# Kernel optimization log

Measured on AMD Instinct MI355X. Metric: run time of the kernel, lower is better.

Reference implementation:

```python
import jax, jax.numpy as jnp
import numpy as np

N, P, D, C = 8192, 512, 2, 4   # queries, coeff grid points, spatial dim, num coefficients
HA = 32                        # attention_net hidden
HP, CP = 32, 16                # pointswise_mlp hidden / output
HG = 256                       # green_function_net hidden


def setup_inputs() -> dict:
    key = jax.random.key(0)
    ks = jax.random.split(key, 16)
    g = lambda k, shp, s: jax.random.normal(k, shp, dtype=jnp.float32) * s
    return {
        "r": g(ks[0], (N, 2 * D), 1.0),
        "r_prime": g(ks[1], (N, 2 * D), 1.0),
        "coeff_x": g(ks[2], (P, D), 1.0),
        "coeff_y": g(ks[3], (P, C), 1.0),
        # attention_net MLP (no bias): concat(q,k)=4 -> 32 -> 32 -> 1
        "Wa1": g(ks[4], (2 * D, HA), 0.5),
        "Wa2": g(ks[5], (HA, HA), 1.0 / np.sqrt(HA)),
        "Wa3": g(ks[6], (HA, 1), 1.0 / np.sqrt(HA)),
        # pointswise_mlp: C -> 32 -> 16
        "Wp1": g(ks[7], (C, HP), 0.5), "bp1": jnp.zeros((HP,), jnp.float32),
        "Wp2": g(ks[8], (HP, CP), 1.0 / np.sqrt(HP)), "bp2": jnp.zeros((CP,), jnp.float32),
        # green_function_net: 4+4+16=24 -> 256 -> 256 -> 1 (exp at the end)
        "Wg1": g(ks[9], (2 * D + 2 * D + CP, HG), 1.0 / np.sqrt(24.0)), "bg1": jnp.zeros((HG,), jnp.float32),
        "Wg2": g(ks[10], (HG, HG), 1.0 / np.sqrt(HG)), "bg2": jnp.zeros((HG,), jnp.float32),
        "Wg3": g(ks[11], (HG, 1), 0.1 / np.sqrt(HG)), "bg3": jnp.zeros((1,), jnp.float32),
    }


def reference(r, r_prime, coeff_x, coeff_y,
              Wa1, Wa2, Wa3, Wp1, bp1, Wp2, bp2,
              Wg1, bg1, Wg2, bg2, Wg3, bg3):
    # --- CoefficientNet: pairwise MLP attention over the coefficient grid ---
    q = r[:, :D]  # (N, 2) spatial position only
    # first layer of attn MLP on concat([q, k]) split into q- and k- parts
    h = jax.nn.relu(q @ Wa1[:D][None if False else slice(None)]  # (N, HA)
                    [..., :] [..., :]  # no-op for readability
                    if False else (q @ Wa1[:D])[:, None, :] + (coeff_x @ Wa1[D:])[None, :, :])  # (N, P, HA)
    h = jax.nn.relu(h @ Wa2)                     # (N, P, HA)
    logits = (h @ Wa3)[..., 0]                   # (N, P)
    attn = jax.nn.softmax(logits, axis=-1)       # (N, P)
    attn_out = attn @ coeff_y                    # (N, C)
    c = jax.nn.relu(attn_out @ Wp1 + bp1) @ Wp2 + bp2  # (N, CP)
    # --- GreenFunctionNet ---
    x = jnp.concatenate([r, r_prime, c], axis=-1)       # (N, 24)
    g1 = jax.nn.relu(x @ Wg1 + bg1)
    g2 = jax.nn.relu(g1 @ Wg2 + bg2)
    return jnp.exp(g2 @ Wg3 + bg3)                      # (N, 1)
```

## Files before the change

kernel.cpp:

```cpp
#include <hip/hip_runtime.h>
#include <math.h>

#define N_ 8192
#define P_ 512

typedef __fp16 half8  __attribute__((ext_vector_type(8)));
typedef __fp16 half2t __attribute__((ext_vector_type(2)));
typedef float  floatx16 __attribute__((ext_vector_type(16)));

union H8 { half8 v; half2t h2[4]; };

static __device__ __forceinline__ half2t pk2(float a, float b) {
    return __builtin_amdgcn_cvt_pkrtz(a, b);
}

#define HP_OFF 17408
#define XS_OFF 21760

__global__ __launch_bounds__(512, 2) void k_fused(
    const float* __restrict__ r,
    const float* __restrict__ rp,
    const float* __restrict__ coeff_x,
    const float* __restrict__ coeff_y,
    const float* __restrict__ Wa1,
    const float* __restrict__ Wa2,
    const float* __restrict__ Wa3,
    const float* __restrict__ Wp1,
    const float* __restrict__ bp1,
    const float* __restrict__ Wp2,
    const float* __restrict__ bp2,
    const float* __restrict__ Wg1,
    const float* __restrict__ bg1,
    const float* __restrict__ Wg2,
    const float* __restrict__ bg2,
    const float* __restrict__ Wg3,
    const float* __restrict__ bg3,
    float* __restrict__ out)
{
    __shared__ __align__(16) unsigned char reg0[49152];
    __shared__ float sA[8][32];
    __shared__ float aoA[4][8][32];
    __shared__ float aoS[32][4];

    const int tid  = threadIdx.x;
    const int n0   = blockIdx.x * 32;
    const int lane = tid & 63;
    const int wv   = tid >> 6;
    const int j32  = lane & 31;
    const int hl   = lane >> 5;
    const int k0g  = hl * 8;

    {
        const float2 cx = ((const float2*)coeff_x)[tid];
        half2t* wrow = (half2t*)(reg0 + tid * 96);
#pragma unroll
        for (int q = 0; q < 16; ++q) {
            const float b0 = cx.x * Wa1[64 + 2*q]     + cx.y * Wa1[96 + 2*q];
            const float b1 = cx.x * Wa1[64 + 2*q + 1] + cx.y * Wa1[96 + 2*q + 1];
            wrow[q] = pk2(b0, b1);
        }
    }

    half2t anh1[4], anh2[4];
    {
        const float2 rv = ((const float2*)r)[2 * (n0 + j32)];
#pragma unroll
        for (int q = 0; q < 4; ++q) {
            const int k1 = k0g + 2*q, k2 = 16 + k0g + 2*q;
            anh1[q] = pk2(rv.x*Wa1[k1]   + rv.y*Wa1[32+k1],
                          rv.x*Wa1[k1+1] + rv.y*Wa1[32+k1+1]);
            anh2[q] = pk2(rv.x*Wa1[k2]   + rv.y*Wa1[32+k2],
                          rv.x*Wa1[k2+1] + rv.y*Wa1[32+k2+1]);
        }
    }
    H8 af1, af2;
#pragma unroll
    for (int q = 0; q < 4; ++q) {
        af1.h2[q] = pk2(Wa2[(k0g + 2*q)     * 32 + j32],
                        Wa2[(k0g + 2*q + 1) * 32 + j32]);
        af2.h2[q] = pk2(Wa2[(16 + k0g + 2*q)     * 32 + j32],
                        Wa2[(16 + k0g + 2*q + 1) * 32 + j32]);
    }
    float w3[16];
#pragma unroll
    for (int g = 0; g < 4; ++g)
#pragma unroll
        for (int i = 0; i < 4; ++i)
            w3[g*4 + i] = Wa3[g*8 + 4*hl + i];

    __syncthreads();

    const half2t zero2 = pk2(0.f, 0.f);
    float s = 0.0f, aox = 0.f, aoy = 0.f, aoz = 0.f, aow = 0.f;

#pragma unroll 2
    for (int pl = 0; pl < 64; ++pl) {
        const int ploc = wv * 64 + pl;
        const half2t* rowq = (const half2t*)(reg0 + ploc * 96) + hl * 4;

        H8 bf1, bf2;
#pragma unroll
        for (int q = 0; q < 4; ++q) {
            bf1.h2[q] = __builtin_elementwise_max(anh1[q] + rowq[q],     zero2);
            bf2.h2[q] = __builtin_elementwise_max(anh2[q] + rowq[8 + q], zero2);
        }

        floatx16 zc = {};
        floatx16 acc = __builtin_amdgcn_mfma_f32_32x32x16_f16(af1.v, bf1.v, zc, 0, 0, 0);
        acc = __builtin_amdgcn_mfma_f32_32x32x16_f16(af2.v, bf2.v, acc, 0, 0, 0);

        float d0 = 0.f, d1 = 0.f, d2 = 0.f, d3 = 0.f;
#pragma unroll
        for (int i = 0; i < 4; ++i) {
            d0 += fmaxf(acc[i],      0.f) * w3[i];
            d1 += fmaxf(acc[4 + i],  0.f) * w3[4 + i];
            d2 += fmaxf(acc[8 + i],  0.f) * w3[8 + i];
            d3 += fmaxf(acc[12 + i], 0.f) * w3[12 + i];
        }
        float dot = (d0 + d1) + (d2 + d3);
        dot += __shfl_xor(dot, 32);

        const float e = __expf(dot);
        const float4 cyv = ((const float4*)coeff_y)[ploc];
        s   += e;
        aox += e * cyv.x;
        aoy += e * cyv.y;
        aoz += e * cyv.z;
        aow += e * cyv.w;
    }

    if (lane < 32) {
        sA[wv][lane]      = s;
        aoA[0][wv][lane]  = aox;
        aoA[1][wv][lane]  = aoy;
        aoA[2][wv][lane]  = aoz;
        aoA[3][wv][lane]  = aow;
    }
    __syncthreads();

    if (tid < 32) {
        float S = 0.f, A0 = 0.f, A1 = 0.f, A2 = 0.f, A3 = 0.f;
#pragma unroll
        for (int w = 0; w < 8; ++w) {
            S  += sA[w][tid];
            A0 += aoA[0][w][tid];
            A1 += aoA[1][w][tid];
            A2 += aoA[2][w][tid];
            A3 += aoA[3][w][tid];
        }
        const float inv = 1.0f / S;
        aoS[tid][0] = A0 * inv;
        aoS[tid][1] = A1 * inv;
        aoS[tid][2] = A2 * inv;
        aoS[tid][3] = A3 * inv;
    }
    __syncthreads();

    float* hpS = (float*)(reg0 + HP_OFF);
    float* xS  = (float*)(reg0 + XS_OFF);
    const int nB = tid & 31;
    const int iB = tid >> 5;

    if (tid < 256) {
        const int nn = tid >> 3, k = tid & 7;
        xS[nn*25 + k] = (k < 4) ? r[(n0+nn)*4 + k] : rp[(n0+nn)*4 + k - 4];
    }
    {
        const float a0 = aoS[nB][0], a1 = aoS[nB][1], a2 = aoS[nB][2], a3 = aoS[nB][3];
#pragma unroll
        for (int rep = 0; rep < 2; ++rep) {
            const int i = iB + rep*16;
            float a = bp1[i] + a0*Wp1[i] + a1*Wp1[32+i] + a2*Wp1[64+i] + a3*Wp1[96+i];
            hpS[nB*33 + i] = fmaxf(a, 0.0f);
        }
    }
    __syncthreads();

    {
        float a = bp2[iB];
#pragma unroll
        for (int i = 0; i < 32; ++i) a += hpS[nB*33 + i] * Wp2[i*16 + iB];
        xS[nB*25 + 8 + iB] = a;
    }
    __syncthreads();

    const int jcol = (wv << 5) + j32;
    __fp16* g1S = (__fp16*)reg0;

    {
        H8 xa1, xa2, wb1, wb2;
        const float* xrow = xS + j32 * 25;
#pragma unroll
        for (int q = 0; q < 4; ++q) {
            xa1.h2[q] = pk2(xrow[k0g + 2*q], xrow[k0g + 2*q + 1]);
            wb1.h2[q] = pk2(Wg1[(k0g + 2*q)*256 + jcol],
                            Wg1[(k0g + 2*q + 1)*256 + jcol]);
            if (hl == 0) {
                xa2.h2[q] = pk2(xrow[16 + 2*q], xrow[16 + 2*q + 1]);
                wb2.h2[q] = pk2(Wg1[(16 + 2*q)*256 + jcol],
                                Wg1[(17 + 2*q)*256 + jcol]);
            } else {
                xa2.h2[q] = pk2(0.f, 0.f);
                wb2.h2[q] = pk2(0.f, 0.f);
            }
        }
        floatx16 g1acc = {};
        g1acc = __builtin_amdgcn_mfma_f32_32x32x16_f16(xa1.v, wb1.v, g1acc, 0, 0, 0);
        g1acc = __builtin_amdgcn_mfma_f32_32x32x16_f16(xa2.v, wb2.v, g1acc, 0, 0, 0);

        const float b1v = bg1[jcol];
#pragma unroll
        for (int i = 0; i < 16; ++i) {
            const int row = (i & 3) + 8*(i >> 2) + 4*hl;
            g1S[row*264 + jcol] = (__fp16)fmaxf(g1acc[i] + b1v, 0.0f);
        }
    }
    __syncthreads();

    {
        H8 wB[16];
#pragma unroll
        for (int kk = 0; kk < 16; ++kk) {
            const int kb = kk*16 + hl*8;
#pragma unroll
            for (int q = 0; q < 4; ++q)
                wB[kk].h2[q] = pk2(Wg2[(kb + 2*q)*256 + jcol],
                                   Wg2[(kb + 2*q + 1)*256 + jcol]);
        }
        floatx16 acc2 = {};
        const __fp16* arow = g1S + j32 * 264;
#pragma unroll
        for (int kk = 0; kk < 16; ++kk) {
            H8 af;
            af.v = *(const half8*)(arow + kk*16 + hl*8);
            acc2 = __builtin_amdgcn_mfma_f32_32x32x16_f16(af.v, wB[kk].v, acc2, 0, 0, 0);
        }

        const float b2v = bg2[jcol];
        const float w3v = Wg3[jcol];
        float part[16];
#pragma unroll
        for (int i = 0; i < 16; ++i)
            part[i] = fmaxf(acc2[i] + b2v, 0.0f) * w3v;
#pragma unroll
        for (int off = 1; off <= 16; off <<= 1) {
#pragma unroll
            for (int i = 0; i < 16; ++i) part[i] += __shfl_xor(part[i], off);
        }
        float* redS = &sA[0][0];
        if ((lane & 31) == 0) {
#pragma unroll
            for (int i = 0; i < 16; ++i) {
                const int row = (i & 3) + 8*(i >> 2) + 4*hl;
                redS[wv*32 + row] = part[i];
            }
        }
        __syncthreads();

        if (tid < 32) {
            float v = bg3[0];
#pragma unroll
            for (int w = 0; w < 8; ++w) v += redS[w*32 + tid];
            out[n0 + tid] = __expf(v);
        }
    }
}

extern "C" void kernel_launch(void* const* d_in, const int* in_sizes, int n_in,
                              void* d_out, int out_size, void* d_ws, size_t ws_size,
                              hipStream_t stream)
{
    const float* r   = (const float*)d_in[0];
    const float* rp  = (const float*)d_in[1];
    const float* cx  = (const float*)d_in[2];
    const float* cy  = (const float*)d_in[3];
    const float* Wa1 = (const float*)d_in[4];
    const float* Wa2 = (const float*)d_in[5];
    const float* Wa3 = (const float*)d_in[6];
    const float* Wp1 = (const float*)d_in[7];
    const float* bp1 = (const float*)d_in[8];
    const float* Wp2 = (const float*)d_in[9];
    const float* bp2 = (const float*)d_in[10];
    const float* Wg1 = (const float*)d_in[11];
    const float* bg1 = (const float*)d_in[12];
    const float* Wg2 = (const float*)d_in[13];
    const float* bg2 = (const float*)d_in[14];
    const float* Wg3 = (const float*)d_in[15];
    const float* bg3 = (const float*)d_in[16];

    hipLaunchKernelGGL(k_fused, dim3(N_/32), dim3(512), 0, stream,
                       r, rp, cx, cy, Wa1, Wa2, Wa3, Wp1, bp1, Wp2, bp2,
                       Wg1, bg1, Wg2, bg2, Wg3, bg3, (float*)d_out);
}
```

Baseline: 112.9 us.

## Split fused kernel into attention and MLP kernels with P-split atomics

Splits the single fused kernel into an attention kernel that divides the 512 coefficient points across two blocks per query tile and combines partial softmax sums with global atomics, followed by a separate kernel for the pointwise and green-function MLPs. This doubles the attention grid to 512 blocks to raise occupancy and parallelism on the CU array. It also caches coeff_y in shared memory and replaces the final attention projection with packed fp16 dot2 instructions. The cost is an extra memset, an extra launch, global atomics, and lower precision in the logit dot product. Partials use unnormalised exp without max subtraction, as before.

```diff
diff --git a/kernel.cpp b/kernel.cpp
--- a/kernel.cpp
+++ b/kernel.cpp
@@ -14,17 +14,148 @@
     return __builtin_amdgcn_cvt_pkrtz(a, b);
 }
 
-#define HP_OFF 17408
-#define XS_OFF 21760
-
-__global__ __launch_bounds__(512, 2) void k_fused(
+__global__ __launch_bounds__(512, 2) void k_attn(
     const float* __restrict__ r,
-    const float* __restrict__ rp,
     const float* __restrict__ coeff_x,
     const float* __restrict__ coeff_y,
     const float* __restrict__ Wa1,
     const float* __restrict__ Wa2,
     const float* __restrict__ Wa3,
+    float* __restrict__ ws_s,
+    float* __restrict__ ws_ao)
+{
+    __shared__ __align__(16) unsigned char bpS[256 * 96];
+    __shared__ __align__(16) float4 cyS[256];
+    __shared__ float sA[8][32];
+    __shared__ float aoA[4][8][32];
+
+    const int tid    = threadIdx.x;
+    const int ntile  = blockIdx.x >> 1;
+    const int pblock = (blockIdx.x & 1) * 256;
+    const int n0     = ntile * 32;
+    const int lane   = tid & 63;
+    const int wv     = tid >> 6;
+    const int j32    = lane & 31;
+    const int hl     = lane >> 5;
+    const int k0g    = hl * 8;
+
+    if (tid < 256) {
+        const float2 cx = ((const float2*)coeff_x)[pblock + tid];
+        half2t* wrow = (half2t*)(bpS + tid * 96);
+#pragma unroll
+        for (int q = 0; q < 16; ++q) {
+            const float b0 = cx.x * Wa1[64 + 2*q]     + cx.y * Wa1[96 + 2*q];
+            const float b1 = cx.x * Wa1[64 + 2*q + 1] + cx.y * Wa1[96 + 2*q + 1];
+            wrow[q] = pk2(b0, b1);
+        }
+    } else {
+        cyS[tid - 256] = ((const float4*)coeff_y)[pblock + tid - 256];
+    }
+
+    half2t anh1[4], anh2[4];
+    {
+        const float2 rv = ((const float2*)r)[2 * (n0 + j32)];
+#pragma unroll
+        for (int q = 0; q < 4; ++q) {
+            const int k1 = k0g + 2*q, k2 = 16 + k0g + 2*q;
+            anh1[q] = pk2(rv.x*Wa1[k1]   + rv.y*Wa1[32+k1],
+                          rv.x*Wa1[k1+1] + rv.y*Wa1[32+k1+1]);
+            anh2[q] = pk2(rv.x*Wa1[k2]   + rv.y*Wa1[32+k2],
+                          rv.x*Wa1[k2+1] + rv.y*Wa1[32+k2+1]);
+        }
+    }
+    H8 af1, af2;
+#pragma unroll
+    for (int q = 0; q < 4; ++q) {
+        af1.h2[q] = pk2(Wa2[(k0g + 2*q)     * 32 + j32],
+                        Wa2[(k0g + 2*q + 1) * 32 + j32]);
+        af2.h2[q] = pk2(Wa2[(16 + k0g + 2*q)     * 32 + j32],
+                        Wa2[(16 + k0g + 2*q + 1) * 32 + j32]);
+    }
+    half2t w3h[8];
+#pragma unroll
+    for (int q = 0; q < 8; ++q) {
+        const int r0 = ((2*q) & 3) + 8*(q >> 1) + 4*hl;
+        w3h[q] = pk2(Wa3[r0], Wa3[r0 + 1]);
+    }
+
+    __syncthreads();
+
+    const half2t zero2 = pk2(0.f, 0.f);
+    float s = 0.0f, aox = 0.f, aoy = 0.f, aoz = 0.f, aow = 0.f;
+
+#pragma unroll 2
+    for (int pl = 0; pl < 32; ++pl) {
+        const int ploc = wv * 32 + pl;
+        const half2t* rowq = (const half2t*)(bpS + ploc * 96) + hl * 4;
+
+        H8 bf1, bf2;
+#pragma unroll
+        for (int q = 0; q < 4; ++q) {
+            bf1.h2[q] = __builtin_elementwise_max(anh1[q] + rowq[q],     zero2);
+            bf2.h2[q] = __builtin_elementwise_max(anh2[q] + rowq[8 + q], zero2);
+        }
+
+        floatx16 zc = {};
+        floatx16 acc = __builtin_amdgcn_mfma_f32_32x32x16_f16(af1.v, bf1.v, zc, 0, 0, 0);
+        acc = __builtin_amdgcn_mfma_f32_32x32x16_f16(af2.v, bf2.v, acc, 0, 0, 0);
+
+        float d0 = 0.f, d1 = 0.f;
+#pragma unroll
+        for (int q = 0; q < 8; q += 2) {
+            half2t z0 = __builtin_elementwise_max(pk2(acc[2*q],   acc[2*q+1]), zero2);
+            half2t z1 = __builtin_elementwise_max(pk2(acc[2*q+2], acc[2*q+3]), zero2);
+            d0 = __builtin_amdgcn_fdot2(z0, w3h[q],   d0, false);
+            d1 = __builtin_amdgcn_fdot2(z1, w3h[q+1], d1, false);
+        }
+        float dot = d0 + d1;
+        dot += __shfl_xor(dot, 32);
+
+        const float e = __expf(dot);
+        const float4 cyv = cyS[ploc];
+        s   += e;
+        aox += e * cyv.x;
+        aoy += e * cyv.y;
+        aoz += e * cyv.z;
+        aow += e * cyv.w;
+    }
+
+    if (lane < 32) {
+        sA[wv][lane]      = s;
+        aoA[0][wv][lane]  = aox;
+        aoA[1][wv][lane]  = aoy;
+        aoA[2][wv][lane]  = aoz;
+        aoA[3][wv][lane]  = aow;
+    }
+    __syncthreads();
+
+    if (tid < 32) {
+        float S = 0.f, A0 = 0.f, A1 = 0.f, A2 = 0.f, A3 = 0.f;
+#pragma unroll
+        for (int w = 0; w < 8; ++w) {
+            S  += sA[w][tid];
+            A0 += aoA[0][w][tid];
+            A1 += aoA[1][w][tid];
+            A2 += aoA[2][w][tid];
+            A3 += aoA[3][w][tid];
+        }
+        const int n = n0 + tid;
+        atomicAdd(ws_s + n, S);
+        atomicAdd(ws_ao + n*4 + 0, A0);
+        atomicAdd(ws_ao + n*4 + 1, A1);
+        atomicAdd(ws_ao + n*4 + 2, A2);
+        atomicAdd(ws_ao + n*4 + 3, A3);
+    }
+}
+
+#define HP_OFF 17408
+#define XS_OFF 21760
+
+__global__ __launch_bounds__(512) void k_rest(
+    const float* __restrict__ r,
+    const float* __restrict__ rp,
+    const float* __restrict__ ws_s,
+    const float* __restrict__ ws_ao,
     const float* __restrict__ Wp1,
     const float* __restrict__ bp1,
     const float* __restrict__ Wp2,
@@ -37,9 +168,8 @@
     const float* __restrict__ bg3,
     float* __restrict__ out)
 {
-    __shared__ __align__(16) unsigned char reg0[49152];
-    __shared__ float sA[8][32];
-    __shared__ float aoA[4][8][32];
+    __shared__ __align__(16) unsigned char reg0[25984];
+    __shared__ float redS[8][32];
     __shared__ float aoS[32][4];
 
     const int tid  = threadIdx.x;
@@ -50,121 +180,23 @@
     const int hl   = lane >> 5;
     const int k0g  = hl * 8;
 
-    {
-        const float2 cx = ((const float2*)coeff_x)[tid];
-        half2t* wrow = (half2t*)(reg0 + tid * 96);
-#pragma unroll
-        for (int q = 0; q < 16; ++q) {
-            const float b0 = cx.x * Wa1[64 + 2*q]     + cx.y * Wa1[96 + 2*q];
-            const float b1 = cx.x * Wa1[64 + 2*q + 1] + cx.y * Wa1[96 + 2*q + 1];
-            wrow[q] = pk2(b0, b1);
-        }
-    }
-
-    half2t anh1[4], anh2[4];
-    {
-        const float2 rv = ((const float2*)r)[2 * (n0 + j32)];
-#pragma unroll
-        for (int q = 0; q < 4; ++q) {
-            const int k1 = k0g + 2*q, k2 = 16 + k0g + 2*q;
-            anh1[q] = pk2(rv.x*Wa1[k1]   + rv.y*Wa1[32+k1],
-                          rv.x*Wa1[k1+1] + rv.y*Wa1[32+k1+1]);
-            anh2[q] = pk2(rv.x*Wa1[k2]   + rv.y*Wa1[32+k2],
-                          rv.x*Wa1[k2+1] + rv.y*Wa1[32+k2+1]);
-        }
-    }
-    H8 af1, af2;
-#pragma unroll
-    for (int q = 0; q < 4; ++q) {
-        af1.h2[q] = pk2(Wa2[(k0g + 2*q)     * 32 + j32],
-                        Wa2[(k0g + 2*q + 1) * 32 + j32]);
-        af2.h2[q] = pk2(Wa2[(16 + k0g + 2*q)     * 32 + j32],
-                        Wa2[(16 + k0g + 2*q + 1) * 32 + j32]);
-    }
-    float w3[16];
-#pragma unroll
-    for (int g = 0; g < 4; ++g)
-#pragma unroll
-        for (int i = 0; i < 4; ++i)
-            w3[g*4 + i] = Wa3[g*8 + 4*hl + i];
-
-    __syncthreads();
-
-    const half2t zero2 = pk2(0.f, 0.f);
-    float s = 0.0f, aox = 0.f, aoy = 0.f, aoz = 0.f, aow = 0.f;
-
-#pragma unroll 2
-    for (int pl = 0; pl < 64; ++pl) {
-        const int ploc = wv * 64 + pl;
-        const half2t* rowq = (const half2t*)(reg0 + ploc * 96) + hl * 4;
-
-        H8 bf1, bf2;
-#pragma unroll
-        for (int q = 0; q < 4; ++q) {
-            bf1.h2[q] = __builtin_elementwise_max(anh1[q] + rowq[q],     zero2);
-            bf2.h2[q] = __builtin_elementwise_max(anh2[q] + rowq[8 + q], zero2);
-        }
-
-        floatx16 zc = {};
-        floatx16 acc = __builtin_amdgcn_mfma_f32_32x32x16_f16(af1.v, bf1.v, zc, 0, 0, 0);
-        acc = __builtin_amdgcn_mfma_f32_32x32x16_f16(af2.v, bf2.v, acc, 0, 0, 0);
-
-        float d0 = 0.f, d1 = 0.f, d2 = 0.f, d3 = 0.f;
-#pragma unroll
-        for (int i = 0; i < 4; ++i) {
-            d0 += fmaxf(acc[i],      0.f) * w3[i];
-            d1 += fmaxf(acc[4 + i],  0.f) * w3[4 + i];
-            d2 += fmaxf(acc[8 + i],  0.f) * w3[8 + i];
-            d3 += fmaxf(acc[12 + i], 0.f) * w3[12 + i];
-        }
-        float dot = (d0 + d1) + (d2 + d3);
-        dot += __shfl_xor(dot, 32);
-
-        const float e = __expf(dot);
-        const float4 cyv = ((const float4*)coeff_y)[ploc];
-        s   += e;
-        aox += e * cyv.x;
-        aoy += e * cyv.y;
-        aoz += e * cyv.z;
-        aow += e * cyv.w;
-    }
-
-    if (lane < 32) {
-        sA[wv][lane]      = s;
-        aoA[0][wv][lane]  = aox;
-        aoA[1][wv][lane]  = aoy;
-        aoA[2][wv][lane]  = aoz;
-        aoA[3][wv][lane]  = aow;
-    }
-    __syncthreads();
-
-    if (tid < 32) {
-        float S = 0.f, A0 = 0.f, A1 = 0.f, A2 = 0.f, A3 = 0.f;
-#pragma unroll
-        for (int w = 0; w < 8; ++w) {
-            S  += sA[w][tid];
-            A0 += aoA[0][w][tid];
-            A1 += aoA[1][w][tid];
-            A2 += aoA[2][w][tid];
-            A3 += aoA[3][w][tid];
-        }
-        const float inv = 1.0f / S;
-        aoS[tid][0] = A0 * inv;
-        aoS[tid][1] = A1 * inv;
-        aoS[tid][2] = A2 * inv;
-        aoS[tid][3] = A3 * inv;
-    }
-    __syncthreads();
-
     float* hpS = (float*)(reg0 + HP_OFF);
     float* xS  = (float*)(reg0 + XS_OFF);
     const int nB = tid & 31;
     const int iB = tid >> 5;
 
+    if (tid < 32) {
+        const float inv = 1.0f / ws_s[n0 + tid];
+#pragma unroll
+        for (int c = 0; c < 4; ++c)
+            aoS[tid][c] = ws_ao[(n0 + tid)*4 + c] * inv;
+    }
     if (tid < 256) {
         const int nn = tid >> 3, k = tid & 7;
         xS[nn*25 + k] = (k < 4) ? r[(n0+nn)*4 + k] : rp[(n0+nn)*4 + k - 4];
     }
+    __syncthreads();
+
     {
         const float a0 = aoS[nB][0], a1 = aoS[nB][1], a2 = aoS[nB][2], a3 = aoS[nB][3];
 #pragma unroll
@@ -186,7 +218,6 @@
 
     const int jcol = (wv << 5) + j32;
     __fp16* g1S = (__fp16*)reg0;
-
     {
         H8 xa1, xa2, wb1, wb2;
         const float* xrow = xS + j32 * 25;
@@ -247,12 +278,11 @@
 #pragma unroll
             for (int i = 0; i < 16; ++i) part[i] += __shfl_xor(part[i], off);
         }
-        float* redS = &sA[0][0];
         if ((lane & 31) == 0) {
 #pragma unroll
             for (int i = 0; i < 16; ++i) {
                 const int row = (i & 3) + 8*(i >> 2) + 4*hl;
-                redS[wv*32 + row] = part[i];
+                redS[wv][row] = part[i];
             }
         }
         __syncthreads();
@@ -260,7 +290,7 @@
         if (tid < 32) {
             float v = bg3[0];
 #pragma unroll
-            for (int w = 0; w < 8; ++w) v += redS[w*32 + tid];
+            for (int w = 0; w < 8; ++w) v += redS[w][tid];
             out[n0 + tid] = __expf(v);
         }
     }
@@ -288,7 +318,14 @@
     const float* Wg3 = (const float*)d_in[15];
     const float* bg3 = (const float*)d_in[16];
 
-    hipLaunchKernelGGL(k_fused, dim3(N_/32), dim3(512), 0, stream,
-                       r, rp, cx, cy, Wa1, Wa2, Wa3, Wp1, bp1, Wp2, bp2,
+    float* ws_s  = (float*)d_ws;
+    float* ws_ao = ws_s + N_;
+
+    (void)hipMemsetAsync(d_ws, 0, (size_t)N_ * 5 * sizeof(float), stream);
+
+    hipLaunchKernelGGL(k_attn, dim3(512),   dim3(512), 0, stream,
+                       r, cx, cy, Wa1, Wa2, Wa3, ws_s, ws_ao);
+    hipLaunchKernelGGL(k_rest, dim3(N_/32), dim3(512), 0, stream,
+                       r, rp, ws_s, ws_ao, Wp1, bp1, Wp2, bp2,
                        Wg1, bg1, Wg2, bg2, Wg3, bg3, (float*)d_out);
 }
```

Result: no change. 113.7 us (+0.7%).

## Raise occupancy target, stage coeff_y in LDS, fp16 dot for logits, chunk Wg2 loads

Applied to the files above, without the earlier changes.

Raises the launch-bounds minimum blocks per CU from 2 to 4, which pushes the compiler to cap registers. To fit that cap, the Wa3 weights become packed fp16 pairs, and the final projection of the attention MLP uses fdot2 on fp16-converted ReLU outputs. coeff_y is staged in shared memory so the inner loop no longer does a global load per iteration. The Wg2 fragment loads are double-buffered in chunks of four instead of holding all sixteen fragments live. Risks are reduced precision in the logits, register spills, and LDS usage limiting how many blocks can actually be resident.

```diff
diff --git a/kernel.cpp b/kernel.cpp
--- a/kernel.cpp
+++ b/kernel.cpp
@@ -17,7 +17,7 @@
 #define HP_OFF 17408
 #define XS_OFF 21760
 
-__global__ __launch_bounds__(512, 2) void k_fused(
+__global__ __launch_bounds__(512, 4) void k_fused(
     const float* __restrict__ r,
     const float* __restrict__ rp,
     const float* __restrict__ coeff_x,
@@ -38,6 +38,7 @@
     float* __restrict__ out)
 {
     __shared__ __align__(16) unsigned char reg0[49152];
+    __shared__ __align__(16) float4 cyS[512];
     __shared__ float sA[8][32];
     __shared__ float aoA[4][8][32];
     __shared__ float aoS[32][4];
@@ -59,18 +60,19 @@
             const float b1 = cx.x * Wa1[64 + 2*q + 1] + cx.y * Wa1[96 + 2*q + 1];
             wrow[q] = pk2(b0, b1);
         }
-    }
-
-    half2t anh1[4], anh2[4];
+        cyS[tid] = ((const float4*)coeff_y)[tid];
+    }
+
+    H8 anh1, anh2;
     {
         const float2 rv = ((const float2*)r)[2 * (n0 + j32)];
 #pragma unroll
         for (int q = 0; q < 4; ++q) {
             const int k1 = k0g + 2*q, k2 = 16 + k0g + 2*q;
-            anh1[q] = pk2(rv.x*Wa1[k1]   + rv.y*Wa1[32+k1],
-                          rv.x*Wa1[k1+1] + rv.y*Wa1[32+k1+1]);
-            anh2[q] = pk2(rv.x*Wa1[k2]   + rv.y*Wa1[32+k2],
-                          rv.x*Wa1[k2+1] + rv.y*Wa1[32+k2+1]);
+            anh1.h2[q] = pk2(rv.x*Wa1[k1]   + rv.y*Wa1[32+k1],
+                             rv.x*Wa1[k1+1] + rv.y*Wa1[32+k1+1]);
+            anh2.h2[q] = pk2(rv.x*Wa1[k2]   + rv.y*Wa1[32+k2],
+                             rv.x*Wa1[k2+1] + rv.y*Wa1[32+k2+1]);
         }
     }
     H8 af1, af2;
@@ -81,12 +83,12 @@
         af2.h2[q] = pk2(Wa2[(16 + k0g + 2*q)     * 32 + j32],
                         Wa2[(16 + k0g + 2*q + 1) * 32 + j32]);
     }
-    float w3[16];
-#pragma unroll
-    for (int g = 0; g < 4; ++g)
-#pragma unroll
-        for (int i = 0; i < 4; ++i)
-            w3[g*4 + i] = Wa3[g*8 + 4*hl + i];
+    half2t w3h[8];
+#pragma unroll
+    for (int q = 0; q < 8; ++q) {
+        const int r0 = ((2*q) & 3) + 8*(q >> 1) + 4*hl;
+        w3h[q] = pk2(Wa3[r0], Wa3[r0 + 1]);
+    }
 
     __syncthreads();
 
@@ -101,27 +103,34 @@
         H8 bf1, bf2;
 #pragma unroll
         for (int q = 0; q < 4; ++q) {
-            bf1.h2[q] = __builtin_elementwise_max(anh1[q] + rowq[q],     zero2);
-            bf2.h2[q] = __builtin_elementwise_max(anh2[q] + rowq[8 + q], zero2);
+            bf1.h2[q] = __builtin_elementwise_max(anh1.h2[q] + rowq[q],     zero2);
+            bf2.h2[q] = __builtin_elementwise_max(anh2.h2[q] + rowq[8 + q], zero2);
         }
 
         floatx16 zc = {};
         floatx16 acc = __builtin_amdgcn_mfma_f32_32x32x16_f16(af1.v, bf1.v, zc, 0, 0, 0);
         acc = __builtin_amdgcn_mfma_f32_32x32x16_f16(af2.v, bf2.v, acc, 0, 0, 0);
 
-        float d0 = 0.f, d1 = 0.f, d2 = 0.f, d3 = 0.f;
-#pragma unroll
-        for (int i = 0; i < 4; ++i) {
-            d0 += fmaxf(acc[i],      0.f) * w3[i];
-            d1 += fmaxf(acc[4 + i],  0.f) * w3[4 + i];
-            d2 += fmaxf(acc[8 + i],  0.f) * w3[8 + i];
-            d3 += fmaxf(acc[12 + i], 0.f) * w3[12 + i];
+        float d0, d1, d2, d3;
+        {
+            half2t z0 = __builtin_elementwise_max(pk2(acc[0],  acc[1]),  zero2);
+            half2t z1 = __builtin_elementwise_max(pk2(acc[2],  acc[3]),  zero2);
+            half2t z2 = __builtin_elementwise_max(pk2(acc[4],  acc[5]),  zero2);
+            half2t z3 = __builtin_elementwise_max(pk2(acc[6],  acc[7]),  zero2);
+            half2t z4 = __builtin_elementwise_max(pk2(acc[8],  acc[9]),  zero2);
+            half2t z5 = __builtin_elementwise_max(pk2(acc[10], acc[11]), zero2);
+            half2t z6 = __builtin_elementwise_max(pk2(acc[12], acc[13]), zero2);
+            half2t z7 = __builtin_elementwise_max(pk2(acc[14], acc[15]), zero2);
+            d0 = __builtin_amdgcn_fdot2(z1, w3h[1], __builtin_amdgcn_fdot2(z0, w3h[0], 0.f, false), false);
+            d1 = __builtin_amdgcn_fdot2(z3, w3h[3], __builtin_amdgcn_fdot2(z2, w3h[2], 0.f, false), false);
+            d2 = __builtin_amdgcn_fdot2(z5, w3h[5], __builtin_amdgcn_fdot2(z4, w3h[4], 0.f, false), false);
+            d3 = __builtin_amdgcn_fdot2(z7, w3h[7], __builtin_amdgcn_fdot2(z6, w3h[6], 0.f, false), false);
         }
         float dot = (d0 + d1) + (d2 + d3);
         dot += __shfl_xor(dot, 32);
 
         const float e = __expf(dot);
-        const float4 cyv = ((const float4*)coeff_y)[ploc];
+        const float4 cyv = cyS[ploc];
         s   += e;
         aox += e * cyv.x;
         aoy += e * cyv.y;
@@ -218,22 +227,38 @@
     __syncthreads();
 
     {
-        H8 wB[16];
-#pragma unroll
-        for (int kk = 0; kk < 16; ++kk) {
-            const int kb = kk*16 + hl*8;
-#pragma unroll
-            for (int q = 0; q < 4; ++q)
-                wB[kk].h2[q] = pk2(Wg2[(kb + 2*q)*256 + jcol],
-                                   Wg2[(kb + 2*q + 1)*256 + jcol]);
-        }
         floatx16 acc2 = {};
         const __fp16* arow = g1S + j32 * 264;
-#pragma unroll
-        for (int kk = 0; kk < 16; ++kk) {
-            H8 af;
-            af.v = *(const half8*)(arow + kk*16 + hl*8);
-            acc2 = __builtin_amdgcn_mfma_f32_32x32x16_f16(af.v, wB[kk].v, acc2, 0, 0, 0);
+
+        H8 wB[4], wBn[4];
+#pragma unroll
+        for (int q = 0; q < 4; ++q) {
+            const int kb = q*16 + hl*8;
+#pragma unroll
+            for (int t = 0; t < 4; ++t)
+                wB[q].h2[t] = pk2(Wg2[(kb + 2*t)*256 + jcol],
+                                  Wg2[(kb + 2*t + 1)*256 + jcol]);
+        }
+#pragma unroll
+        for (int c = 0; c < 4; ++c) {
+            if (c < 3) {
+#pragma unroll
+                for (int q = 0; q < 4; ++q) {
+                    const int kb = (c*4 + 4 + q)*16 + hl*8;
+#pragma unroll
+                    for (int t = 0; t < 4; ++t)
+                        wBn[q].h2[t] = pk2(Wg2[(kb + 2*t)*256 + jcol],
+                                           Wg2[(kb + 2*t + 1)*256 + jcol]);
+                }
+            }
+#pragma unroll
+            for (int q = 0; q < 4; ++q) {
+                H8 af;
+                af.v = *(const half8*)(arow + (c*4 + q)*16 + hl*8);
+                acc2 = __builtin_amdgcn_mfma_f32_32x32x16_f16(af.v, wB[q].v, acc2, 0, 0, 0);
+            }
+#pragma unroll
+            for (int q = 0; q < 4; ++q) wB[q] = wBn[q];
         }
 
         const float b2v = bg2[jcol];
```

Result: faster. 110.2 us (-2.4%).
